# Optimization experiments

Measured on AMD Instinct MI355X. Metric: run time of the kernel, lower is better.

## Reference

```python
import jax, jax.numpy as jnp
import numpy as np

B, IN, H = 8192, 1024, 2048

def setup_inputs() -> dict:
    key = jax.random.key(0)
    k1, k2, k3, k4, k5 = jax.random.split(key, 5)
    prev_state = jax.random.normal(k1, (B, H), dtype=jnp.float32)
    x = jax.random.normal(k2, (B, IN), dtype=jnp.float32)
    input_weights = jax.random.normal(k3, (H, IN), dtype=jnp.float32) / IN ** 0.5
    input_bias = jnp.zeros((H,), dtype=jnp.float32)
    recurrent_weights = jax.random.normal(k4, (H, H), dtype=jnp.float32) / H ** 0.5
    U_z = jax.random.normal(k5, (H, H), dtype=jnp.float32) / H ** 0.5
    b_u = jnp.zeros((H,), dtype=jnp.float32)
    return {"prev_state": prev_state, "input": x,
            "input_weights": input_weights, "input_bias": input_bias,
            "recurrent_weights": recurrent_weights, "U_z": U_z, "b_u": b_u}

def reference(prev_state, input, input_weights, input_bias, recurrent_weights, U_z, b_u):
    # z = tanh(x @ W_x^T + b_x)
    z = jnp.tanh(input @ input_weights.T + input_bias)
    # u = sigmoid(h @ W_h^T + z @ U_z^T + b_u)
    u = jax.nn.sigmoid(prev_state @ recurrent_weights.T + z @ U_z.T + b_u)
    # convex combination of previous state and candidate
    state = u * prev_state + (1.0 - u) * z
    return state
```

## Files before the change

### kernel.cpp

```cpp
#include <hip/hip_runtime.h>
#include <hip/hip_bf16.h>
#include <cstdint>
#include <cstddef>

#define DEVFN static __device__ __forceinline__

typedef __attribute__((ext_vector_type(8))) short bf16x8;
typedef __attribute__((ext_vector_type(4))) float f32x4;

static constexpr int kB = 8192;
static constexpr int kIN = 1024;
static constexpr int kH = 2048;

DEVFN unsigned short f32_to_bf16(float f) {
  union { float f; unsigned int u; } v; v.f = f;
  unsigned int x = v.u;
  x += 0x7fffu + ((x >> 16) & 1u);
  return (unsigned short)(x >> 16);
}
DEVFN float bf16_to_f32(unsigned short u) {
  union { unsigned int u; float f; } v; v.u = (unsigned int)u << 16;
  return v.f;
}

__global__ void cast_all(const float* __restrict__ x, const float* __restrict__ Wx,
                         const float* __restrict__ Wh, const float* __restrict__ Uz,
                         const float* __restrict__ h,
                         unsigned short* __restrict__ xb, unsigned short* __restrict__ Wxb,
                         unsigned short* __restrict__ Wcat, unsigned short* __restrict__ Acat) {
  const long i = (long)blockIdx.x * blockDim.x + threadIdx.x;
  const float* src; unsigned short* dst; int sh, stride, off; long li;
  if (i < 2097152L)      { li = i;            src = x;  dst = xb;   sh = 8; stride = 1024; off = 0; }
  else if (i < 2621440L) { li = i - 2097152L; src = Wx; dst = Wxb;  sh = 8; stride = 1024; off = 0; }
  else if (i < 3670016L) { li = i - 2621440L; src = Wh; dst = Wcat; sh = 9; stride = 4096; off = 0; }
  else if (i < 4718592L) { li = i - 3670016L; src = Uz; dst = Wcat; sh = 9; stride = 4096; off = 2048; }
  else                   { li = i - 4718592L; src = h;  dst = Acat; sh = 9; stride = 4096; off = 0; }
  float4 v = *(const float4*)(src + li * 4);
  const long row = li >> sh;
  const long col = (li & ((1L << sh) - 1)) * 4;
  unsigned short* d = dst + row * stride + off + col;
  ushort4 o;
  o.x = f32_to_bf16(v.x); o.y = f32_to_bf16(v.y);
  o.z = f32_to_bf16(v.z); o.w = f32_to_bf16(v.w);
  *(ushort4*)d = o;
}

typedef const __attribute__((address_space(1))) unsigned int* gptr_t;
typedef __attribute__((address_space(3))) unsigned int* lptr_t;
DEVFN void gload16(const unsigned short* g, unsigned short* l) {
  __builtin_amdgcn_global_load_lds((gptr_t)g, (lptr_t)l, 16, 0, 0);
}

DEVFN void bar() { __builtin_amdgcn_s_barrier(); }
#define LGKM0() asm volatile("s_waitcnt lgkmcnt(0)" ::: "memory")
#define VMC6()  asm volatile("s_waitcnt vmcnt(6)" ::: "memory")


template<int BUF, int QM>
DEVFN void ldA(bf16x8 (&a)[4][2], const unsigned short* lds, int wm, int lr, int lg) {
  const unsigned short* rg = lds + (size_t)(BUF * 4 + wm) * 8192;
#pragma unroll
  for (int mi = 0; mi < 4; ++mi) {
    const int rl = QM * 64 + mi * 16 + lr;
#pragma unroll
    for (int kk = 0; kk < 2; ++kk) {
      const int kel = (kk * 32 + lg * 8) ^ ((rl & 7) * 8);
      a[mi][kk] = *(const bf16x8*)(rg + rl * 64 + kel);
    }
  }
}

template<int BUF, int QN>
DEVFN void ldB(bf16x8 (&b)[4][2], const unsigned short* lds, int wn, int lr, int lg) {
  const unsigned short* rg = lds + (size_t)(BUF * 4 + 2 + (wn >> 1)) * 8192;
#pragma unroll
  for (int ni = 0; ni < 2; ++ni) {
    const int n = QN * 2 + ni;
    const int cl = (wn & 1) * 64 + n * 16 + lr;
#pragma unroll
    for (int kk = 0; kk < 2; ++kk) {
      const int kel = (kk * 32 + lg * 8) ^ ((cl & 7) * 8);
      b[n][kk] = *(const bf16x8*)(rg + cl * 64 + kel);
    }
  }
}

template<int QM, int QN>
DEVFN void mfmaQ(f32x4 (&acc)[8][4], bf16x8 (&a)[4][2], bf16x8 (&b)[4][2]) {
  __builtin_amdgcn_s_setprio(1);
#pragma unroll
  for (int mi = 0; mi < 4; ++mi)
#pragma unroll
    for (int ni = 0; ni < 2; ++ni)
#pragma unroll
      for (int kk = 0; kk < 2; ++kk)
        acc[QM * 4 + mi][QN * 2 + ni] = __builtin_amdgcn_mfma_f32_16x16x32_bf16(
            a[mi][kk], b[QN * 2 + ni][kk], acc[QM * 4 + mi][QN * 2 + ni], 0, 0, 0);
  __builtin_amdgcn_s_setprio(0);
}

template<int EPI>
__global__ __launch_bounds__(512, 1)
void gemm256(const unsigned short* __restrict__ A,
             const unsigned short* __restrict__ W,
             const float* __restrict__ bias,
             int M, int K,
             unsigned short* __restrict__ zOut,
             const unsigned short* __restrict__ hzBuf, int ldhz,
             float* __restrict__ out, int ldo)
{
  __shared__ unsigned short lds[8][8192];
  unsigned short* L = &lds[0][0];

  const int nTM = M >> 8;
  const int bm = blockIdx.x % nTM, bn = blockIdx.x / nTM;
  const int rowBase = bm << 8, colBase = bn << 8;

  const int t = threadIdx.x;
  const int l = t & 63;
  const int w = t >> 6;
  const int lr = l & 15, lg = l >> 4;
  const int wm = w >> 2, wn = w & 3;

  const int srow = t >> 3;
  const int scol = (t & 7) * 8;
  const int kcSrc = scol ^ ((srow & 7) * 8);
  const unsigned short* gA = A + (size_t)(rowBase + srow) * K + kcSrc;
  const unsigned short* gB = W + (size_t)(colBase + srow) * K + kcSrc;

#define STAGE(BUF, OP, HALF, KT) do {                                          \
    const unsigned short* gs = ((OP) ? gB : gA)                                \
        + (size_t)((HALF) * 128) * K + (size_t)(KT) * 64;                      \
    unsigned short* ld = L + (size_t)((BUF) * 4 + (OP) * 2 + (HALF)) * 8192    \
        + w * 512;                                                             \
    gload16(gs, ld);                                                           \
    gload16(gs + (size_t)64 * K, ld + 4096);                                   \
  } while (0)

  f32x4 acc[8][4] = {};
  bf16x8 a[4][2], b[4][2];

  STAGE(0, 0, 0, 0); STAGE(0, 0, 1, 0); STAGE(0, 1, 0, 0); STAGE(0, 1, 1, 0);
  STAGE(1, 1, 0, 1); STAGE(1, 1, 1, 1); STAGE(1, 0, 0, 1);
  VMC6();
  bar();

  const int NP = K >> 7;
  for (int i = 0; i < NP; ++i) {
    const bool more = (i + 1 < NP);
    const int ktb1 = 2 * i + 1;
    const int kt0n = more ? 2 * i + 2 : 2 * i;
    const int kt1n = more ? 2 * i + 3 : 2 * i + 1;

    ldA<0, 0>(a, L, wm, lr, lg); ldB<0, 0>(b, L, wn, lr, lg);
    STAGE(1, 0, 1, ktb1);
    bar(); LGKM0();
    mfmaQ<0, 0>(acc, a, b);
    bar();
    ldB<0, 1>(b, L, wn, lr, lg);
    bar(); LGKM0();
    mfmaQ<0, 1>(acc, a, b);
    bar();
    ldA<0, 1>(a, L, wm, lr, lg);
    STAGE(0, 1, 0, kt0n);
    bar(); LGKM0();
    mfmaQ<1, 0>(acc, a, b);
    bar();
    STAGE(0, 1, 1, kt0n);
    STAGE(0, 0, 0, kt0n);
    bar(); LGKM0();
    mfmaQ<1, 1>(acc, a, b);
    VMC6();
    bar();
    ldA<1, 0>(a, L, wm, lr, lg); ldB<1, 0>(b, L, wn, lr, lg);
    STAGE(0, 0, 1, kt0n);
    bar(); LGKM0();
    mfmaQ<0, 0>(acc, a, b);
    bar();
    ldB<1, 1>(b, L, wn, lr, lg);
    bar(); LGKM0();
    mfmaQ<0, 1>(acc, a, b);
    bar();
    ldA<1, 1>(a, L, wm, lr, lg);
    STAGE(1, 1, 0, kt1n);
    bar(); LGKM0();
    mfmaQ<1, 0>(acc, a, b);
    bar();
    STAGE(1, 1, 1, kt1n);
    STAGE(1, 0, 0, kt1n);
    bar(); LGKM0();
    mfmaQ<1, 1>(acc, a, b);
    VMC6();
    bar();
  }
#undef STAGE

#pragma unroll
  for (int m = 0; m < 8; ++m) {
    const int r0 = rowBase + wm * 128 + m * 16 + lg * 4;
#pragma unroll
    for (int n = 0; n < 4; ++n) {
      const int c = colBase + wn * 64 + n * 16 + lr;
      const float bs = bias[c];
#pragma unroll
      for (int q = 0; q < 4; ++q) {
        const int r = r0 + q;
        const float pre = acc[m][n][q] + bs;
        if (EPI == 0) {
          zOut[(size_t)r * ldhz + c] = f32_to_bf16(tanhf(pre));
        } else {
          const float u = 1.0f / (1.0f + __expf(-pre));
          const float hv = bf16_to_f32(hzBuf[(size_t)r * ldhz + c]);
          const float zv = bf16_to_f32(hzBuf[(size_t)r * ldhz + 2048 + c]);
          out[(size_t)r * ldo + c] = u * hv + (1.0f - u) * zv;
        }
      }
    }
  }
}

extern "C" void kernel_launch(void* const* d_in, const int* in_sizes, int n_in,
                              void* d_out, int out_size, void* d_ws, size_t ws_size,
                              hipStream_t stream) {
  const float* h  = (const float*)d_in[0];
  const float* x  = (const float*)d_in[1];
  const float* Wx = (const float*)d_in[2];
  const float* bx = (const float*)d_in[3];
  const float* Wh = (const float*)d_in[4];
  const float* Uz = (const float*)d_in[5];
  const float* bu = (const float*)d_in[6];
  float* out = (float*)d_out;

  unsigned short* ws   = (unsigned short*)d_ws;
  unsigned short* xb   = ws;
  unsigned short* Wxb  = xb + (size_t)kB * kIN;
  unsigned short* Wcat = Wxb + (size_t)kH * kIN;
  unsigned short* Acat = Wcat + (size_t)kH * 2 * kH;

  cast_all<<<34816, 256, 0, stream>>>(x, Wx, Wh, Uz, h, xb, Wxb, Wcat, Acat);

  const int grid = (kB / 256) * (kH / 256);

  gemm256<0><<<grid, 512, 0, stream>>>(
      xb, Wxb, bx, kB, kIN, Acat + kH, nullptr, 2 * kH, nullptr, 0);

  gemm256<1><<<grid, 512, 0, stream>>>(
      Acat, Wcat, bu, kB, 2 * kH, nullptr, Acat, 2 * kH, out, kH);
}
```

Measured before the change: 213.9 us.

## Software-pipeline LDS fragment loads one quarter ahead of MFMA blocks

Restructures the GEMM main loop so the LDS reads for the next MFMA quarter are issued before or alongside the current quarter's MFMAs, instead of loading and then waiting with explicit lgkmcnt(0) before each quarter. The prologue now stages all eight tiles and waits for them to complete, and the in-loop global-load waits change from vmcnt(6) to vmcnt(2) with barriers moved. The aim is to hide LDS latency behind matrix math and cut stall points. In exchange it relies on compiler-inserted waits for correctness, and because fragment registers are overwritten while the same registers feed pending MFMAs, the new ordering carries a risk of LDS read/write hazards.

```diff
diff --git a/kernel.cpp b/kernel.cpp
--- a/kernel.cpp
+++ b/kernel.cpp
@@ -52,8 +52,8 @@
 }
 
 DEVFN void bar() { __builtin_amdgcn_s_barrier(); }
-#define LGKM0() asm volatile("s_waitcnt lgkmcnt(0)" ::: "memory")
-#define VMC6()  asm volatile("s_waitcnt vmcnt(6)" ::: "memory")
+#define VMC0() asm volatile("s_waitcnt vmcnt(0)" ::: "memory")
+#define VMC2() asm volatile("s_waitcnt vmcnt(2)" ::: "memory")
 
 
 template<int BUF, int QM>
@@ -140,57 +140,61 @@
   f32x4 acc[8][4] = {};
   bf16x8 a[4][2], b[4][2];
 
-  STAGE(0, 0, 0, 0); STAGE(0, 0, 1, 0); STAGE(0, 1, 0, 0); STAGE(0, 1, 1, 0);
-  STAGE(1, 1, 0, 1); STAGE(1, 1, 1, 1); STAGE(1, 0, 0, 1);
-  VMC6();
+  STAGE(0, 1, 0, 0); STAGE(0, 1, 1, 0); STAGE(0, 0, 0, 0); STAGE(0, 0, 1, 0);
+  STAGE(1, 1, 0, 1); STAGE(1, 1, 1, 1); STAGE(1, 0, 0, 1); STAGE(1, 0, 1, 1);
+  VMC0();
   bar();
+  ldA<0, 0>(a, L, wm, lr, lg);
+  ldB<0, 0>(b, L, wn, lr, lg);
 
   const int NP = K >> 7;
-  for (int i = 0; i < NP; ++i) {
-    const bool more = (i + 1 < NP);
-    const int ktb1 = 2 * i + 1;
-    const int kt0n = more ? 2 * i + 2 : 2 * i;
-    const int kt1n = more ? 2 * i + 3 : 2 * i + 1;
-
-    ldA<0, 0>(a, L, wm, lr, lg); ldB<0, 0>(b, L, wn, lr, lg);
+  for (int j = 0; j < NP; ++j) {
+    const bool more = (j + 1 < NP);
+    const int ktb1 = 2 * j + 1;
+    const int kt0n = more ? 2 * j + 2 : 2 * j;
+    const int kt1n = more ? 2 * j + 3 : 2 * j + 1;
+
+    ldB<0, 1>(b, L, wn, lr, lg);
     STAGE(1, 0, 1, ktb1);
-    bar(); LGKM0();
+    bar();
     mfmaQ<0, 0>(acc, a, b);
     bar();
-    ldB<0, 1>(b, L, wn, lr, lg);
-    bar(); LGKM0();
+    bar();
     mfmaQ<0, 1>(acc, a, b);
-    bar();
     ldA<0, 1>(a, L, wm, lr, lg);
+    bar();
     STAGE(0, 1, 0, kt0n);
-    bar(); LGKM0();
+    bar();
     mfmaQ<1, 0>(acc, a, b);
-    bar();
+    VMC2();
+    bar();
+    ldB<1, 0>(b, L, wn, lr, lg);
     STAGE(0, 1, 1, kt0n);
+    bar();
+    mfmaQ<1, 1>(acc, a, b);
+    ldA<1, 0>(a, L, wm, lr, lg);
+    bar();
+    ldB<1, 1>(b, L, wn, lr, lg);
     STAGE(0, 0, 0, kt0n);
-    bar(); LGKM0();
-    mfmaQ<1, 1>(acc, a, b);
-    VMC6();
-    bar();
-    ldA<1, 0>(a, L, wm, lr, lg); ldB<1, 0>(b, L, wn, lr, lg);
+    bar();
+    mfmaQ<0, 0>(acc, a, b);
+    bar();
     STAGE(0, 0, 1, kt0n);
-    bar(); LGKM0();
-    mfmaQ<0, 0>(acc, a, b);
-    bar();
-    ldB<1, 1>(b, L, wn, lr, lg);
-    bar(); LGKM0();
+    bar();
     mfmaQ<0, 1>(acc, a, b);
-    bar();
     ldA<1, 1>(a, L, wm, lr, lg);
+    bar();
     STAGE(1, 1, 0, kt1n);
-    bar(); LGKM0();
+    bar();
     mfmaQ<1, 0>(acc, a, b);
-    bar();
+    VMC2();
+    bar();
+    ldB<0, 0>(b, L, wn, lr, lg);
     STAGE(1, 1, 1, kt1n);
     STAGE(1, 0, 0, kt1n);
-    bar(); LGKM0();
+    bar();
     mfmaQ<1, 1>(acc, a, b);
-    VMC6();
+    ldA<0, 0>(a, L, wm, lr, lg);
     bar();
   }
 #undef STAGE
```

After: 206.1 us (median of 2 runs). -3.7%, faster.
